# Performance work log

Measured on AMD Instinct MI355X. Metric: run time of the kernel, lower is better.

Reference implementation:

```python
import jax, jax.numpy as jnp
import numpy as np

EPS = 1e-5
N, E, IN, H, EA, T, L = 20000, 80000, 64, 32, 32, 64, 3


def graph_norm(h, w, b, ms):
    # PyG GraphNorm over a single graph: per-feature mean/var over all nodes
    mean = jnp.mean(h, axis=0, keepdims=True)
    out = h - ms * mean
    var = jnp.mean(out * out, axis=0, keepdims=True)
    return out / jnp.sqrt(var + EPS) * w + b


def setup_inputs() -> dict:
    key = jax.random.key(0)
    ks = jax.random.split(key, 24)
    s = 0.05
    inp = {
        'x': jax.random.normal(ks[0], (N, IN), jnp.float32),
        'edge_attr': jax.random.uniform(ks[1], (E, EA), dtype=jnp.float32),
        'edge_index': jax.random.randint(ks[2], (2, E), 0, N, jnp.int32),
        # initial projection in_dim -> hidden
        'init_W': jax.random.normal(ks[3], (IN, H), jnp.float32) * s,
        'init_b': jnp.zeros((H,), jnp.float32),
        # per-layer edge MLP: edge_attr_dim -> H*H (then ReLU)
        'edge_mlp_W': jax.random.normal(ks[4], (L, EA, H * H), jnp.float32) * s,
        'edge_mlp_b': jnp.zeros((L, H * H), jnp.float32),
        # NNConv root weight and bias
        'root_W': jax.random.normal(ks[5], (L, H, H), jnp.float32) * s,
        'root_b': jnp.zeros((L, H), jnp.float32),
        # per-layer GraphNorm params
        'gn_w': jnp.ones((L, H), jnp.float32),
        'gn_b': jnp.zeros((L, H), jnp.float32),
        'gn_ms': jnp.ones((L, H), jnp.float32),
        # per-layer dense transition: 2H -> H
        'trans_W': jax.random.normal(ks[6], (L, 2 * H, H), jnp.float32) * s,
        'trans_b': jnp.zeros((L, H), jnp.float32),
        # final transition H -> T and final GraphNorm
        'final_W': jax.random.normal(ks[7], (H, T), jnp.float32) * s,
        'final_b': jnp.zeros((T,), jnp.float32),
        'fgn_w': jnp.ones((T,), jnp.float32),
        'fgn_b': jnp.zeros((T,), jnp.float32),
        'fgn_ms': jnp.ones((T,), jnp.float32),
    }
    return inp


def reference(x, edge_attr, edge_index, init_W, init_b, edge_mlp_W, edge_mlp_b,
              root_W, root_b, gn_w, gn_b, gn_ms, trans_W, trans_b,
              final_W, final_b, fgn_w, fgn_b, fgn_ms):
    src, dst = edge_index[0], edge_index[1]
    n_nodes = x.shape[0]
    h = x @ init_W + init_b  # [N, H]
    for i in range(L):
        # edge-conditioned per-edge weight matrices [E, H, H]
        ew = jax.nn.relu(edge_attr @ edge_mlp_W[i] + edge_mlp_b[i]).reshape(-1, H, H)
        # gather source node feats, per-edge matmul, scatter-add to targets
        msg = jnp.einsum('ei,eio->eo', h[src], ew)  # [E, H]
        agg = jax.ops.segment_sum(msg, dst, num_segments=n_nodes)
        conv = agg + h @ root_W[i] + root_b[i]
        # GraphNorm + ReLU + residual (in_channels == out_channels)
        hc = jax.nn.relu(graph_norm(conv, gn_w[i], gn_b[i], gn_ms[i])) + h
        # dense transition on [h, h_conv]
        h = jax.nn.relu(jnp.concatenate([h, hc], axis=1) @ trans_W[i] + trans_b[i])
    out = h @ final_W + final_b
    return jax.nn.relu(graph_norm(out, fgn_w, fgn_b, fgn_ms))
```

## Files before the change

kernel.cpp:

```cpp
#include <hip/hip_runtime.h>

namespace {

constexpr int kN  = 20000;
constexpr int kE  = 80000;
constexpr int kIn = 64;
constexpr int kH  = 32;
constexpr int kEA = 32;
constexpr int kT  = 64;
constexpr int kL  = 3;
constexpr float kEps = 1e-5f;

typedef __attribute__((ext_vector_type(8))) short bf16x8;
typedef __attribute__((ext_vector_type(4))) float f32x4;

__device__ inline unsigned short f2bf(float f) {
  unsigned u = __builtin_bit_cast(unsigned, f);
  unsigned r = (u + 0x7fff + ((u >> 16) & 1)) >> 16;
  return (unsigned short)r;
}
__device__ inline float bf2f(unsigned short s) {
  unsigned u = ((unsigned)s) << 16;
  return __builtin_bit_cast(float, u);
}

__global__ __launch_bounds__(256) void hist_dst(const int* __restrict__ ei,
                                                int* __restrict__ cnt) {
  const int e = blockIdx.x * 256 + threadIdx.x;
  if (e < kE) atomicAdd(&cnt[ei[kE + e]], 1);
}

__global__ __launch_bounds__(1024) void scan_nodes(const int* __restrict__ cnt,
                                                   int* __restrict__ off,
                                                   int* __restrict__ cursor) {
  __shared__ int wsum[16];
  __shared__ int woff[16];
  const int tid = threadIdx.x, lane = tid & 63, wid = tid >> 6;
  constexpr int CH = 20;
  const int base = tid * CH;
  int v[CH];
  int s = 0;
#pragma unroll
  for (int j = 0; j < CH; ++j) {
    const int i = base + j;
    const int c = (i < kN) ? cnt[i] : 0;
    v[j] = s;
    s += c;
  }
  int x = s;
#pragma unroll
  for (int d = 1; d < 64; d <<= 1) {
    int y = __shfl_up(x, d);
    if (lane >= d) x += y;
  }
  if (lane == 63) wsum[wid] = x;
  __syncthreads();
  if (tid < 16) {
    int t = wsum[tid];
    int xx = t;
#pragma unroll
    for (int d = 1; d < 16; d <<= 1) {
      int y = __shfl_up(xx, d);
      if (tid >= d) xx += y;
    }
    woff[tid] = xx - t;
  }
  __syncthreads();
  const int thrbase = woff[wid] + (x - s);
#pragma unroll
  for (int j = 0; j < CH; ++j) {
    const int i = base + j;
    if (i < kN) {
      off[i] = thrbase + v[j];
      cursor[i] = thrbase + v[j];
    }
  }
}

__global__ __launch_bounds__(256) void place_edges(const int* __restrict__ ei,
                                                   int* __restrict__ cursor,
                                                   int* __restrict__ pos) {
  const int e = blockIdx.x * 256 + threadIdx.x;
  if (e < kE) pos[e] = atomicAdd(&cursor[ei[kE + e]], 1);
}

__global__ __launch_bounds__(256) void pack_w(const float* __restrict__ emW,
                                              unsigned short* __restrict__ wbf) {
  const int idx = blockIdx.x * 256 + threadIdx.x;
  if (idx >= kL * 64 * 64) return;
  const int lane = idx & 63, ct = (idx >> 6) & 63, l = idx >> 12;
  const int k0 = (lane >> 4) * 8, c = ct * 16 + (lane & 15);
  const float* W = emW + (size_t)l * kEA * kH * kH;
  unsigned out[4];
#pragma unroll
  for (int p = 0; p < 4; ++p) {
    unsigned lo = f2bf(W[(size_t)(k0 + 2 * p) * (kH * kH) + c]);
    unsigned hi = f2bf(W[(size_t)(k0 + 2 * p + 1) * (kH * kH) + c]);
    out[p] = lo | (hi << 16);
  }
  *reinterpret_cast<uint4*>(wbf + (size_t)idx * 8) =
      make_uint4(out[0], out[1], out[2], out[3]);
}

__global__ __launch_bounds__(64) void init_proj(
    const float* __restrict__ x, const float* __restrict__ W,
    const float* __restrict__ b, float* __restrict__ h) {
  __shared__ float Wl[kIn * kH];
  __shared__ float bl[kH];
  const int tid = threadIdx.x;
  {
    const float4* Ws = reinterpret_cast<const float4*>(W);
    float4* Wd = reinterpret_cast<float4*>(Wl);
    for (int j = tid; j < kIn * kH / 4; j += 64) Wd[j] = Ws[j];
  }
  if (tid < kH) bl[tid] = b[tid];
  __syncthreads();
  const int node = blockIdx.x * 64 + tid;
  if (node >= kN) return;
  float xr[kIn];
  const float4* xp = reinterpret_cast<const float4*>(x + (size_t)node * kIn);
#pragma unroll
  for (int k4 = 0; k4 < kIn / 4; ++k4) {
    float4 v = xp[k4];
    xr[k4 * 4 + 0] = v.x; xr[k4 * 4 + 1] = v.y;
    xr[k4 * 4 + 2] = v.z; xr[k4 * 4 + 3] = v.w;
  }
  float* hp = h + (size_t)node * kH;
#pragma unroll
  for (int o = 0; o < kH; ++o) {
    float acc = bl[o];
#pragma unroll
    for (int k = 0; k < kIn; ++k) acc = fmaf(xr[k], Wl[k * kH + o], acc);
    hp[o] = acc;
  }
}

constexpr int HP  = 40;
constexpr int MPW = 36;
__global__ __launch_bounds__(256) void edge_msg_mfma(
    const float* __restrict__ attr, const int* __restrict__ ei,
    const int* __restrict__ pos, const float* __restrict__ h,
    const unsigned short* __restrict__ wbf, const float* __restrict__ bm,
    float* __restrict__ msg_buf) {
  __shared__ float bml[kH * kH];
  __shared__ unsigned short hbuf[4][32 * HP];
  __shared__ float mbuf[4][32 * MPW];
  const int tid = threadIdx.x;
  const int wv = tid >> 6, lane = tid & 63;
  const int lr = lane & 15, lg = lane >> 4;
  const int base = (blockIdx.x * 4 + wv) * 32;

  for (int j = tid; j < kH * kH; j += 256) bml[j] = bm[j];

  bf16x8 AfA, AfB;
  {
    const float4* ap = reinterpret_cast<const float4*>(
        attr + (size_t)(base + lr) * kEA + lg * 8);
    float4 a0 = ap[0], a1 = ap[1];
    AfA[0] = (short)f2bf(a0.x); AfA[1] = (short)f2bf(a0.y);
    AfA[2] = (short)f2bf(a0.z); AfA[3] = (short)f2bf(a0.w);
    AfA[4] = (short)f2bf(a1.x); AfA[5] = (short)f2bf(a1.y);
    AfA[6] = (short)f2bf(a1.z); AfA[7] = (short)f2bf(a1.w);
    const float4* bp = reinterpret_cast<const float4*>(
        attr + (size_t)(base + 16 + lr) * kEA + lg * 8);
    float4 b0 = bp[0], b1 = bp[1];
    AfB[0] = (short)f2bf(b0.x); AfB[1] = (short)f2bf(b0.y);
    AfB[2] = (short)f2bf(b0.z); AfB[3] = (short)f2bf(b0.w);
    AfB[4] = (short)f2bf(b1.x); AfB[5] = (short)f2bf(b1.y);
    AfB[6] = (short)f2bf(b1.z); AfB[7] = (short)f2bf(b1.w);
  }

  for (int c = lane; c < 128; c += 64) {
    const int er = c >> 2, q = c & 3;
    const int src = ei[base + er];
    const float4* hp4 =
        reinterpret_cast<const float4*>(h + (size_t)src * kH + q * 8);
    float4 h0 = hp4[0], h1 = hp4[1];
    uint2 p0 = make_uint2(f2bf(h0.x) | ((unsigned)f2bf(h0.y) << 16),
                          f2bf(h0.z) | ((unsigned)f2bf(h0.w) << 16));
    uint2 p1 = make_uint2(f2bf(h1.x) | ((unsigned)f2bf(h1.y) << 16),
                          f2bf(h1.z) | ((unsigned)f2bf(h1.w) << 16));
    *reinterpret_cast<uint2*>(&hbuf[wv][0] + er * HP + q * 8) = p0;
    *reinterpret_cast<uint2*>(&hbuf[wv][0] + er * HP + q * 8 + 4) = p1;
  }

  __syncthreads();

  float maA[4][2] = {{0.f, 0.f}, {0.f, 0.f}, {0.f, 0.f}, {0.f, 0.f}};
  float maB[4][2] = {{0.f, 0.f}, {0.f, 0.f}, {0.f, 0.f}, {0.f, 0.f}};
  const unsigned short* hrow = &hbuf[wv][0];

#pragma unroll
  for (int g = 0; g < 4; ++g) {
    bf16x8 hA0 = *reinterpret_cast<const bf16x8*>(hrow + (lg * 4 + 0) * HP + g * 8);
    bf16x8 hA1 = *reinterpret_cast<const bf16x8*>(hrow + (lg * 4 + 1) * HP + g * 8);
    bf16x8 hA2 = *reinterpret_cast<const bf16x8*>(hrow + (lg * 4 + 2) * HP + g * 8);
    bf16x8 hA3 = *reinterpret_cast<const bf16x8*>(hrow + (lg * 4 + 3) * HP + g * 8);
    bf16x8 hB0 = *reinterpret_cast<const bf16x8*>(hrow + (16 + lg * 4 + 0) * HP + g * 8);
    bf16x8 hB1 = *reinterpret_cast<const bf16x8*>(hrow + (16 + lg * 4 + 1) * HP + g * 8);
    bf16x8 hB2 = *reinterpret_cast<const bf16x8*>(hrow + (16 + lg * 4 + 2) * HP + g * 8);
    bf16x8 hB3 = *reinterpret_cast<const bf16x8*>(hrow + (16 + lg * 4 + 3) * HP + g * 8);
#pragma unroll
    for (int i8 = 0; i8 < 8; ++i8) {
      const int il = g * 8 + i8;
      bf16x8 B0 = *reinterpret_cast<const bf16x8*>(
          wbf + ((size_t)(il * 2 + 0) * 64 + lane) * 8);
      bf16x8 B1 = *reinterpret_cast<const bf16x8*>(
          wbf + ((size_t)(il * 2 + 1) * 64 + lane) * 8);
      const float b0 = bml[il * kH + lr];
      const float b1 = bml[il * kH + 16 + lr];
      f32x4 c0A, c1A, c0B, c1B;
      c0A[0] = b0; c0A[1] = b0; c0A[2] = b0; c0A[3] = b0;
      c1A[0] = b1; c1A[1] = b1; c1A[2] = b1; c1A[3] = b1;
      c0B = c0A; c1B = c1A;
      c0A = __builtin_amdgcn_mfma_f32_16x16x32_bf16(AfA, B0, c0A, 0, 0, 0);
      c1A = __builtin_amdgcn_mfma_f32_16x16x32_bf16(AfA, B1, c1A, 0, 0, 0);
      c0B = __builtin_amdgcn_mfma_f32_16x16x32_bf16(AfB, B0, c0B, 0, 0, 0);
      c1B = __builtin_amdgcn_mfma_f32_16x16x32_bf16(AfB, B1, c1B, 0, 0, 0);
      {
        const float h0 = bf2f((unsigned short)hA0[i8]);
        const float h1 = bf2f((unsigned short)hA1[i8]);
        const float h2 = bf2f((unsigned short)hA2[i8]);
        const float h3 = bf2f((unsigned short)hA3[i8]);
        maA[0][0] = fmaf(fmaxf(c0A[0], 0.f), h0, maA[0][0]);
        maA[1][0] = fmaf(fmaxf(c0A[1], 0.f), h1, maA[1][0]);
        maA[2][0] = fmaf(fmaxf(c0A[2], 0.f), h2, maA[2][0]);
        maA[3][0] = fmaf(fmaxf(c0A[3], 0.f), h3, maA[3][0]);
        maA[0][1] = fmaf(fmaxf(c1A[0], 0.f), h0, maA[0][1]);
        maA[1][1] = fmaf(fmaxf(c1A[1], 0.f), h1, maA[1][1]);
        maA[2][1] = fmaf(fmaxf(c1A[2], 0.f), h2, maA[2][1]);
        maA[3][1] = fmaf(fmaxf(c1A[3], 0.f), h3, maA[3][1]);
      }
      {
        const float h0 = bf2f((unsigned short)hB0[i8]);
        const float h1 = bf2f((unsigned short)hB1[i8]);
        const float h2 = bf2f((unsigned short)hB2[i8]);
        const float h3 = bf2f((unsigned short)hB3[i8]);
        maB[0][0] = fmaf(fmaxf(c0B[0], 0.f), h0, maB[0][0]);
        maB[1][0] = fmaf(fmaxf(c0B[1], 0.f), h1, maB[1][0]);
        maB[2][0] = fmaf(fmaxf(c0B[2], 0.f), h2, maB[2][0]);
        maB[3][0] = fmaf(fmaxf(c0B[3], 0.f), h3, maB[3][0]);
        maB[0][1] = fmaf(fmaxf(c1B[0], 0.f), h0, maB[0][1]);
        maB[1][1] = fmaf(fmaxf(c1B[1], 0.f), h1, maB[1][1]);
        maB[2][1] = fmaf(fmaxf(c1B[2], 0.f), h2, maB[2][1]);
        maB[3][1] = fmaf(fmaxf(c1B[3], 0.f), h3, maB[3][1]);
      }
    }
  }

  float* mrow = &mbuf[wv][0];
#pragma unroll
  for (int r = 0; r < 4; ++r) {
    mrow[(lg * 4 + r) * MPW + lr] = maA[r][0];
    mrow[(lg * 4 + r) * MPW + 16 + lr] = maA[r][1];
    mrow[(16 + lg * 4 + r) * MPW + lr] = maB[r][0];
    mrow[(16 + lg * 4 + r) * MPW + 16 + lr] = maB[r][1];
  }
  for (int c = lane; c < 128; c += 64) {
    const int er = c >> 2, q = c & 3;
    const int mp = pos[base + er];
    float4 v0 = *reinterpret_cast<const float4*>(mrow + er * MPW + q * 8);
    float4 v1 = *reinterpret_cast<const float4*>(mrow + er * MPW + q * 8 + 4);
    float* orow = msg_buf + (size_t)mp * kH + q * 8;
    *reinterpret_cast<float4*>(orow) = v0;
    *reinterpret_cast<float4*>(orow + 4) = v1;
  }
}

__global__ __launch_bounds__(256) void agg_root_stats(
    const float* __restrict__ msg, const int* __restrict__ off,
    const int* __restrict__ cnt, const float* __restrict__ h,
    const float* __restrict__ W, const float* __restrict__ b,
    float* __restrict__ conv, float* __restrict__ stats) {
  __shared__ float Wl[kH * kH];
  __shared__ float bl[kH];
  __shared__ float buf[256 * (kH + 1)];
  const int tid = threadIdx.x;
  {
    const float4* Ws = reinterpret_cast<const float4*>(W);
    float4* Wd = reinterpret_cast<float4*>(Wl);
    if (tid < kH * kH / 4) Wd[tid] = Ws[tid];
  }
  if (tid < kH) bl[tid] = b[tid];
  __syncthreads();
  const int node = blockIdx.x * 256 + tid;
  const bool act = node < kN;
  float acc[kH];
#pragma unroll
  for (int o = 0; o < kH; ++o) acc[o] = 0.f;
  if (act) {
#pragma unroll
    for (int o = 0; o < kH; ++o) acc[o] = bl[o];
    const int s = off[node], c = cnt[node];
    for (int j = 0; j < c; ++j) {
      const float4* mp =
          reinterpret_cast<const float4*>(msg + (size_t)(s + j) * kH);
#pragma unroll
      for (int o4 = 0; o4 < kH / 4; ++o4) {
        float4 v = mp[o4];
        acc[o4 * 4 + 0] += v.x; acc[o4 * 4 + 1] += v.y;
        acc[o4 * 4 + 2] += v.z; acc[o4 * 4 + 3] += v.w;
      }
    }
    float hr[kH];
    const float4* hp = reinterpret_cast<const float4*>(h + (size_t)node * kH);
#pragma unroll
    for (int i4 = 0; i4 < kH / 4; ++i4) {
      float4 v = hp[i4];
      hr[i4 * 4 + 0] = v.x; hr[i4 * 4 + 1] = v.y;
      hr[i4 * 4 + 2] = v.z; hr[i4 * 4 + 3] = v.w;
    }
#pragma unroll
    for (int o = 0; o < kH; ++o) {
      float a = acc[o];
#pragma unroll
      for (int i = 0; i < kH; ++i) a = fmaf(hr[i], Wl[i * kH + o], a);
      acc[o] = a;
    }
    float* cp = conv + (size_t)node * kH;
#pragma unroll
    for (int o4 = 0; o4 < kH / 4; ++o4)
      *reinterpret_cast<float4*>(cp + o4 * 4) =
          make_float4(acc[o4 * 4], acc[o4 * 4 + 1], acc[o4 * 4 + 2],
                      acc[o4 * 4 + 3]);
  }
#pragma unroll
  for (int o = 0; o < kH; ++o) buf[tid * (kH + 1) + o] = act ? acc[o] : 0.f;
  __syncthreads();
  if (tid < kH) {
    float s = 0.f, q = 0.f;
#pragma unroll 8
    for (int r = 0; r < 256; ++r) {
      float v = buf[r * (kH + 1) + tid];
      s += v;
      q = fmaf(v, v, q);
    }
    atomicAdd(stats + tid, s);
    atomicAdd(stats + kH + tid, q);
  }
}

__global__ __launch_bounds__(64) void norm_trans(
    const float* __restrict__ conv, const float* __restrict__ stats,
    const float* __restrict__ gw, const float* __restrict__ gb,
    const float* __restrict__ gms, const float* __restrict__ Wt,
    const float* __restrict__ tb, float* __restrict__ h) {
  __shared__ float Wl[2 * kH * kH];
  __shared__ float tbl[kH];
  __shared__ float meanl[kH], rstdl[kH], gwl[kH], gbl[kH];
  const int tid = threadIdx.x;
  {
    const float4* Ws = reinterpret_cast<const float4*>(Wt);
    float4* Wd = reinterpret_cast<float4*>(Wl);
    for (int j = tid; j < 2 * kH * kH / 4; j += 64) Wd[j] = Ws[j];
  }
  if (tid < kH) {
    tbl[tid] = tb[tid];
    float m = stats[tid] * (1.f / kN);
    float q = stats[kH + tid] * (1.f / kN);
    float msv = gms[tid];
    float var = q - m * m * msv * (2.f - msv);
    meanl[tid] = msv * m;
    rstdl[tid] = rsqrtf(var + kEps);
    gwl[tid] = gw[tid];
    gbl[tid] = gb[tid];
  }
  __syncthreads();
  const int node = blockIdx.x * 64 + tid;
  if (node >= kN) return;
  float in_[2 * kH];
  const float* hp = h + (size_t)node * kH;
  const float* cp = conv + (size_t)node * kH;
#pragma unroll
  for (int i = 0; i < kH; ++i) in_[i] = hp[i];
#pragma unroll
  for (int o = 0; o < kH; ++o) {
    float v = cp[o];
    in_[kH + o] =
        fmaxf((v - meanl[o]) * rstdl[o] * gwl[o] + gbl[o], 0.f) + in_[o];
  }
  float* hw = h + (size_t)node * kH;
#pragma unroll
  for (int o = 0; o < kH; ++o) {
    float acc = tbl[o];
#pragma unroll
    for (int k = 0; k < 2 * kH; ++k) acc = fmaf(in_[k], Wl[k * kH + o], acc);
    hw[o] = fmaxf(acc, 0.f);
  }
}

__global__ __launch_bounds__(64) void final_lin(
    const float* __restrict__ h, const float* __restrict__ W,
    const float* __restrict__ b, float* __restrict__ out,
    float* __restrict__ stats) {
  __shared__ float Wl[kH * kT];
  __shared__ float bl[kT];
  __shared__ float buf[64 * (kT + 1)];
  const int tid = threadIdx.x;
  {
    const float4* Ws = reinterpret_cast<const float4*>(W);
    float4* Wd = reinterpret_cast<float4*>(Wl);
    for (int j = tid; j < kH * kT / 4; j += 64) Wd[j] = Ws[j];
  }
  if (tid < kT) bl[tid] = b[tid];
  __syncthreads();
  const int node = blockIdx.x * 64 + tid;
  const bool act = node < kN;
  float hr[kH];
  if (act) {
    const float4* hp = reinterpret_cast<const float4*>(h + (size_t)node * kH);
#pragma unroll
    for (int i4 = 0; i4 < kH / 4; ++i4) {
      float4 v = hp[i4];
      hr[i4 * 4 + 0] = v.x; hr[i4 * 4 + 1] = v.y;
      hr[i4 * 4 + 2] = v.z; hr[i4 * 4 + 3] = v.w;
    }
  } else {
#pragma unroll
    for (int i = 0; i < kH; ++i) hr[i] = 0.f;
  }
  float* op = out + (size_t)node * kT;
#pragma unroll
  for (int o = 0; o < kT; ++o) {
    float acc = 0.f;
    if (act) {
      acc = bl[o];
#pragma unroll
      for (int i = 0; i < kH; ++i) acc = fmaf(hr[i], Wl[i * kT + o], acc);
      op[o] = acc;
    }
    buf[tid * (kT + 1) + o] = act ? acc : 0.f;
  }
  __syncthreads();
  if (tid < kT) {
    float s = 0.f, q = 0.f;
#pragma unroll 8
    for (int r = 0; r < 64; ++r) {
      float v = buf[r * (kT + 1) + tid];
      s += v;
      q = fmaf(v, v, q);
    }
    atomicAdd(stats + tid, s);
    atomicAdd(stats + kT + tid, q);
  }
}

__global__ __launch_bounds__(64) void final_norm(
    const float* __restrict__ stats, const float* __restrict__ w,
    const float* __restrict__ b, const float* __restrict__ ms,
    float* __restrict__ out) {
  __shared__ float meanl[kT], rstdl[kT], wl2[kT], bl2[kT];
  const int tid = threadIdx.x;
  if (tid < kT) {
    float m = stats[tid] * (1.f / kN);
    float q = stats[kT + tid] * (1.f / kN);
    float msv = ms[tid];
    float var = q - m * m * msv * (2.f - msv);
    meanl[tid] = msv * m;
    rstdl[tid] = rsqrtf(var + kEps);
    wl2[tid] = w[tid];
    bl2[tid] = b[tid];
  }
  __syncthreads();
  const int node = blockIdx.x * 64 + tid;
  if (node >= kN) return;
  float* op = out + (size_t)node * kT;
#pragma unroll
  for (int o4 = 0; o4 < kT / 4; ++o4) {
    float4 v = *reinterpret_cast<const float4*>(op + o4 * 4);
    float r[4] = {v.x, v.y, v.z, v.w};
#pragma unroll
    for (int j = 0; j < 4; ++j) {
      int o = o4 * 4 + j;
      r[j] = fmaxf((r[j] - meanl[o]) * rstdl[o] * wl2[o] + bl2[o], 0.f);
    }
    *reinterpret_cast<float4*>(op + o4 * 4) =
        make_float4(r[0], r[1], r[2], r[3]);
  }
}

}

extern "C" void kernel_launch(void* const* d_in, const int* in_sizes, int n_in,
                              void* d_out, int out_size, void* d_ws,
                              size_t ws_size, hipStream_t stream) {
  const float* x     = (const float*)d_in[0];
  const float* eattr = (const float*)d_in[1];
  const int*   eidx  = (const int*)d_in[2];
  const float* initW = (const float*)d_in[3];
  const float* initb = (const float*)d_in[4];
  const float* emW   = (const float*)d_in[5];
  const float* emb   = (const float*)d_in[6];
  const float* rW    = (const float*)d_in[7];
  const float* rb    = (const float*)d_in[8];
  const float* gnw   = (const float*)d_in[9];
  const float* gnb   = (const float*)d_in[10];
  const float* gnms  = (const float*)d_in[11];
  const float* tW    = (const float*)d_in[12];
  const float* tb    = (const float*)d_in[13];
  const float* fW    = (const float*)d_in[14];
  const float* fb    = (const float*)d_in[15];
  const float* fgw   = (const float*)d_in[16];
  const float* fgb   = (const float*)d_in[17];
  const float* fgms  = (const float*)d_in[18];
  float* out = (float*)d_out;

  float* h     = (float*)d_ws;
  float* conv  = h + (size_t)kN * kH;
  float* stats = conv + (size_t)kN * kH;
  float* msg   = stats + 512;
  unsigned short* wbf = (unsigned short*)(msg + (size_t)kE * kH);
  int* cnt    = (int*)(wbf + (size_t)kL * 64 * 64 * 8);
  int* off    = cnt + kN;
  int* cursor = off + kN;
  int* pos    = cursor + kN;

  const int node64  = (kN + 63) / 64;
  const int node256 = (kN + 255) / 256;
  const int edgeBlocks = kE / 128;

  hipMemsetAsync(cnt, 0, kN * sizeof(int), stream);
  hipMemsetAsync(stats, 0, 512 * sizeof(float), stream);
  hist_dst<<<(kE + 255) / 256, 256, 0, stream>>>(eidx, cnt);
  scan_nodes<<<1, 1024, 0, stream>>>(cnt, off, cursor);
  place_edges<<<(kE + 255) / 256, 256, 0, stream>>>(eidx, cursor, pos);

  pack_w<<<kL * 64 * 64 / 256, 256, 0, stream>>>(emW, wbf);
  init_proj<<<node64, 64, 0, stream>>>(x, initW, initb, h);
  for (int l = 0; l < kL; ++l) {
    float* st = stats + l * 128;
    edge_msg_mfma<<<edgeBlocks, 256, 0, stream>>>(
        eattr, eidx, pos, h, wbf + (size_t)l * 64 * 64 * 8,
        emb + (size_t)l * kH * kH, msg);
    agg_root_stats<<<node256, 256, 0, stream>>>(
        msg, off, cnt, h, rW + (size_t)l * kH * kH, rb + l * kH, conv, st);
    norm_trans<<<node64, 64, 0, stream>>>(
        conv, st, gnw + l * kH, gnb + l * kH, gnms + l * kH,
        tW + (size_t)l * 2 * kH * kH, tb + l * kH, h);
  }
  final_lin<<<node64, 64, 0, stream>>>(h, fW, fb, out, stats + 3 * 128);
  final_norm<<<node64, 64, 0, stream>>>(stats + 3 * 128, fgw, fgb, fgms, out);
}
```

Measured before the change: 238.5 us.

## Remap node kernels to one thread per output feature with shuffle broadcasts

The node-level kernels (init_proj, agg_root_stats, norm_trans, final_lin, final_norm) switch from one thread per node with large per-thread register arrays to one lane per output feature. Groups of 32 (or 64) lanes handle a node, and input features are broadcast with __shfl. Global loads and stores become coalesced across lanes, register pressure drops, and the per-block stats reduction moves from a large padded shared buffer to shared-memory atomics. In exchange, each node's edge aggregation loop now runs per lane, and the shuffle-based inner product adds cross-lane traffic.

```diff
diff --git a/kernel.cpp b/kernel.cpp
--- a/kernel.cpp
+++ b/kernel.cpp
@@ -102,7 +102,7 @@
       make_uint4(out[0], out[1], out[2], out[3]);
 }
 
-__global__ __launch_bounds__(64) void init_proj(
+__global__ __launch_bounds__(256) void init_proj(
     const float* __restrict__ x, const float* __restrict__ W,
     const float* __restrict__ b, float* __restrict__ h) {
   __shared__ float Wl[kIn * kH];
@@ -111,27 +111,23 @@
   {
     const float4* Ws = reinterpret_cast<const float4*>(W);
     float4* Wd = reinterpret_cast<float4*>(Wl);
-    for (int j = tid; j < kIn * kH / 4; j += 64) Wd[j] = Ws[j];
+    for (int j = tid; j < kIn * kH / 4; j += 256) Wd[j] = Ws[j];
   }
   if (tid < kH) bl[tid] = b[tid];
   __syncthreads();
-  const int node = blockIdx.x * 64 + tid;
-  if (node >= kN) return;
-  float xr[kIn];
-  const float4* xp = reinterpret_cast<const float4*>(x + (size_t)node * kIn);
-#pragma unroll
-  for (int k4 = 0; k4 < kIn / 4; ++k4) {
-    float4 v = xp[k4];
-    xr[k4 * 4 + 0] = v.x; xr[k4 * 4 + 1] = v.y;
-    xr[k4 * 4 + 2] = v.z; xr[k4 * 4 + 3] = v.w;
-  }
-  float* hp = h + (size_t)node * kH;
-#pragma unroll
-  for (int o = 0; o < kH; ++o) {
+  const int hw = tid >> 5, o = tid & 31;
+#pragma unroll
+  for (int k = 0; k < 4; ++k) {
+    const int node = blockIdx.x * 32 + hw + 8 * k;
+    const float xa = x[(size_t)node * kIn + o];
+    const float xb = x[(size_t)node * kIn + 32 + o];
     float acc = bl[o];
 #pragma unroll
-    for (int k = 0; k < kIn; ++k) acc = fmaf(xr[k], Wl[k * kH + o], acc);
-    hp[o] = acc;
+    for (int i = 0; i < 32; ++i) {
+      acc = fmaf(__shfl(xa, i, 32), Wl[i * kH + o], acc);
+      acc = fmaf(__shfl(xb, i, 32), Wl[(32 + i) * kH + o], acc);
+    }
+    h[(size_t)node * kH + o] = acc;
   }
 }
 
@@ -274,7 +270,7 @@
     float* __restrict__ conv, float* __restrict__ stats) {
   __shared__ float Wl[kH * kH];
   __shared__ float bl[kH];
-  __shared__ float buf[256 * (kH + 1)];
+  __shared__ float ssum[2 * kH];
   const int tid = threadIdx.x;
   {
     const float4* Ws = reinterpret_cast<const float4*>(W);
@@ -282,65 +278,31 @@
     if (tid < kH * kH / 4) Wd[tid] = Ws[tid];
   }
   if (tid < kH) bl[tid] = b[tid];
-  __syncthreads();
-  const int node = blockIdx.x * 256 + tid;
-  const bool act = node < kN;
-  float acc[kH];
-#pragma unroll
-  for (int o = 0; o < kH; ++o) acc[o] = 0.f;
-  if (act) {
-#pragma unroll
-    for (int o = 0; o < kH; ++o) acc[o] = bl[o];
+  if (tid < 2 * kH) ssum[tid] = 0.f;
+  __syncthreads();
+  const int hw = tid >> 5, o = tid & 31;
+  float sreg = 0.f, qreg = 0.f;
+#pragma unroll
+  for (int k = 0; k < 4; ++k) {
+    const int node = blockIdx.x * 32 + hw + 8 * k;
+    float acc = bl[o];
     const int s = off[node], c = cnt[node];
-    for (int j = 0; j < c; ++j) {
-      const float4* mp =
-          reinterpret_cast<const float4*>(msg + (size_t)(s + j) * kH);
-#pragma unroll
-      for (int o4 = 0; o4 < kH / 4; ++o4) {
-        float4 v = mp[o4];
-        acc[o4 * 4 + 0] += v.x; acc[o4 * 4 + 1] += v.y;
-        acc[o4 * 4 + 2] += v.z; acc[o4 * 4 + 3] += v.w;
-      }
-    }
-    float hr[kH];
-    const float4* hp = reinterpret_cast<const float4*>(h + (size_t)node * kH);
-#pragma unroll
-    for (int i4 = 0; i4 < kH / 4; ++i4) {
-      float4 v = hp[i4];
-      hr[i4 * 4 + 0] = v.x; hr[i4 * 4 + 1] = v.y;
-      hr[i4 * 4 + 2] = v.z; hr[i4 * 4 + 3] = v.w;
-    }
-#pragma unroll
-    for (int o = 0; o < kH; ++o) {
-      float a = acc[o];
-#pragma unroll
-      for (int i = 0; i < kH; ++i) a = fmaf(hr[i], Wl[i * kH + o], a);
-      acc[o] = a;
-    }
-    float* cp = conv + (size_t)node * kH;
-#pragma unroll
-    for (int o4 = 0; o4 < kH / 4; ++o4)
-      *reinterpret_cast<float4*>(cp + o4 * 4) =
-          make_float4(acc[o4 * 4], acc[o4 * 4 + 1], acc[o4 * 4 + 2],
-                      acc[o4 * 4 + 3]);
-  }
-#pragma unroll
-  for (int o = 0; o < kH; ++o) buf[tid * (kH + 1) + o] = act ? acc[o] : 0.f;
-  __syncthreads();
-  if (tid < kH) {
-    float s = 0.f, q = 0.f;
-#pragma unroll 8
-    for (int r = 0; r < 256; ++r) {
-      float v = buf[r * (kH + 1) + tid];
-      s += v;
-      q = fmaf(v, v, q);
-    }
-    atomicAdd(stats + tid, s);
-    atomicAdd(stats + kH + tid, q);
-  }
-}
-
-__global__ __launch_bounds__(64) void norm_trans(
+    for (int j = 0; j < c; ++j) acc += msg[(size_t)(s + j) * kH + o];
+    const float hself = h[(size_t)node * kH + o];
+#pragma unroll
+    for (int i = 0; i < kH; ++i)
+      acc = fmaf(__shfl(hself, i, 32), Wl[i * kH + o], acc);
+    conv[(size_t)node * kH + o] = acc;
+    sreg += acc;
+    qreg = fmaf(acc, acc, qreg);
+  }
+  atomicAdd(&ssum[o], sreg);
+  atomicAdd(&ssum[kH + o], qreg);
+  __syncthreads();
+  if (tid < 2 * kH) atomicAdd(stats + tid, ssum[tid]);
+}
+
+__global__ __launch_bounds__(256) void norm_trans(
     const float* __restrict__ conv, const float* __restrict__ stats,
     const float* __restrict__ gw, const float* __restrict__ gb,
     const float* __restrict__ gms, const float* __restrict__ Wt,
@@ -352,7 +314,7 @@
   {
     const float4* Ws = reinterpret_cast<const float4*>(Wt);
     float4* Wd = reinterpret_cast<float4*>(Wl);
-    for (int j = tid; j < 2 * kH * kH / 4; j += 64) Wd[j] = Ws[j];
+    for (int j = tid; j < 2 * kH * kH / 4; j += 256) Wd[j] = Ws[j];
   }
   if (tid < kH) {
     tbl[tid] = tb[tid];
@@ -366,86 +328,61 @@
     gbl[tid] = gb[tid];
   }
   __syncthreads();
-  const int node = blockIdx.x * 64 + tid;
-  if (node >= kN) return;
-  float in_[2 * kH];
-  const float* hp = h + (size_t)node * kH;
-  const float* cp = conv + (size_t)node * kH;
-#pragma unroll
-  for (int i = 0; i < kH; ++i) in_[i] = hp[i];
-#pragma unroll
-  for (int o = 0; o < kH; ++o) {
-    float v = cp[o];
-    in_[kH + o] =
-        fmaxf((v - meanl[o]) * rstdl[o] * gwl[o] + gbl[o], 0.f) + in_[o];
-  }
-  float* hw = h + (size_t)node * kH;
-#pragma unroll
-  for (int o = 0; o < kH; ++o) {
+  const int hw = tid >> 5, o = tid & 31;
+#pragma unroll
+  for (int k = 0; k < 4; ++k) {
+    const int node = blockIdx.x * 32 + hw + 8 * k;
+    const float hv = h[(size_t)node * kH + o];
+    const float cv = conv[(size_t)node * kH + o];
+    const float hc =
+        fmaxf((cv - meanl[o]) * rstdl[o] * gwl[o] + gbl[o], 0.f) + hv;
     float acc = tbl[o];
 #pragma unroll
-    for (int k = 0; k < 2 * kH; ++k) acc = fmaf(in_[k], Wl[k * kH + o], acc);
-    hw[o] = fmaxf(acc, 0.f);
-  }
-}
-
-__global__ __launch_bounds__(64) void final_lin(
+    for (int i = 0; i < kH; ++i) {
+      acc = fmaf(__shfl(hv, i, 32), Wl[i * kH + o], acc);
+      acc = fmaf(__shfl(hc, i, 32), Wl[(kH + i) * kH + o], acc);
+    }
+    h[(size_t)node * kH + o] = fmaxf(acc, 0.f);
+  }
+}
+
+__global__ __launch_bounds__(256) void final_lin(
     const float* __restrict__ h, const float* __restrict__ W,
     const float* __restrict__ b, float* __restrict__ out,
     float* __restrict__ stats) {
   __shared__ float Wl[kH * kT];
   __shared__ float bl[kT];
-  __shared__ float buf[64 * (kT + 1)];
+  __shared__ float ssum[2 * kT];
   const int tid = threadIdx.x;
   {
     const float4* Ws = reinterpret_cast<const float4*>(W);
     float4* Wd = reinterpret_cast<float4*>(Wl);
-    for (int j = tid; j < kH * kT / 4; j += 64) Wd[j] = Ws[j];
+    for (int j = tid; j < kH * kT / 4; j += 256) Wd[j] = Ws[j];
   }
   if (tid < kT) bl[tid] = b[tid];
-  __syncthreads();
-  const int node = blockIdx.x * 64 + tid;
-  const bool act = node < kN;
-  float hr[kH];
-  if (act) {
-    const float4* hp = reinterpret_cast<const float4*>(h + (size_t)node * kH);
-#pragma unroll
-    for (int i4 = 0; i4 < kH / 4; ++i4) {
-      float4 v = hp[i4];
-      hr[i4 * 4 + 0] = v.x; hr[i4 * 4 + 1] = v.y;
-      hr[i4 * 4 + 2] = v.z; hr[i4 * 4 + 3] = v.w;
-    }
-  } else {
-#pragma unroll
-    for (int i = 0; i < kH; ++i) hr[i] = 0.f;
-  }
-  float* op = out + (size_t)node * kT;
-#pragma unroll
-  for (int o = 0; o < kT; ++o) {
-    float acc = 0.f;
-    if (act) {
-      acc = bl[o];
-#pragma unroll
-      for (int i = 0; i < kH; ++i) acc = fmaf(hr[i], Wl[i * kT + o], acc);
-      op[o] = acc;
-    }
-    buf[tid * (kT + 1) + o] = act ? acc : 0.f;
-  }
-  __syncthreads();
-  if (tid < kT) {
-    float s = 0.f, q = 0.f;
-#pragma unroll 8
-    for (int r = 0; r < 64; ++r) {
-      float v = buf[r * (kT + 1) + tid];
-      s += v;
-      q = fmaf(v, v, q);
-    }
-    atomicAdd(stats + tid, s);
-    atomicAdd(stats + kT + tid, q);
-  }
-}
-
-__global__ __launch_bounds__(64) void final_norm(
+  if (tid < 2 * kT) ssum[tid] = 0.f;
+  __syncthreads();
+  const int wv = tid >> 6, o = tid & 63;
+  float sreg = 0.f, qreg = 0.f;
+#pragma unroll
+  for (int k = 0; k < 8; ++k) {
+    const int node = blockIdx.x * 32 + wv + 4 * k;
+    const float hself = h[(size_t)node * kH + (o & 31)];
+    float acc = bl[o];
+#pragma unroll
+    for (int i = 0; i < kH; ++i)
+      acc = fmaf(__shfl(hself, i, 32), Wl[i * kT + o], acc);
+    out[(size_t)node * kT + o] = acc;
+    sreg += acc;
+    qreg = fmaf(acc, acc, qreg);
+  }
+  atomicAdd(&ssum[o], sreg);
+  atomicAdd(&ssum[kT + o], qreg);
+  __syncthreads();
+  if (tid < 2 * kT) atomicAdd(stats + tid, ssum[tid]);
+}
+
+__global__ __launch_bounds__(256) void final_norm(
     const float* __restrict__ stats, const float* __restrict__ w,
     const float* __restrict__ b, const float* __restrict__ ms,
     float* __restrict__ out) {
@@ -462,21 +399,17 @@
     bl2[tid] = b[tid];
   }
   __syncthreads();
-  const int node = blockIdx.x * 64 + tid;
-  if (node >= kN) return;
-  float* op = out + (size_t)node * kT;
-#pragma unroll
-  for (int o4 = 0; o4 < kT / 4; ++o4) {
-    float4 v = *reinterpret_cast<const float4*>(op + o4 * 4);
-    float r[4] = {v.x, v.y, v.z, v.w};
-#pragma unroll
-    for (int j = 0; j < 4; ++j) {
-      int o = o4 * 4 + j;
-      r[j] = fmaxf((r[j] - meanl[o]) * rstdl[o] * wl2[o] + bl2[o], 0.f);
-    }
-    *reinterpret_cast<float4*>(op + o4 * 4) =
-        make_float4(r[0], r[1], r[2], r[3]);
-  }
+  const int idx = blockIdx.x * 256 + tid;
+  const int f = idx * 4;
+  const int c0 = f & 63;
+  float4 v = *reinterpret_cast<const float4*>(out + f);
+  float r[4] = {v.x, v.y, v.z, v.w};
+#pragma unroll
+  for (int j = 0; j < 4; ++j) {
+    const int o = c0 + j;
+    r[j] = fmaxf((r[j] - meanl[o]) * rstdl[o] * wl2[o] + bl2[o], 0.f);
+  }
+  *reinterpret_cast<float4*>(out + f) = make_float4(r[0], r[1], r[2], r[3]);
 }
 
 }
@@ -515,8 +448,7 @@
   int* cursor = off + kN;
   int* pos    = cursor + kN;
 
-  const int node64  = (kN + 63) / 64;
-  const int node256 = (kN + 255) / 256;
+  const int nodeHW  = kN / 32;
   const int edgeBlocks = kE / 128;
 
   hipMemsetAsync(cnt, 0, kN * sizeof(int), stream);
@@ -526,18 +458,19 @@
   place_edges<<<(kE + 255) / 256, 256, 0, stream>>>(eidx, cursor, pos);
 
   pack_w<<<kL * 64 * 64 / 256, 256, 0, stream>>>(emW, wbf);
-  init_proj<<<node64, 64, 0, stream>>>(x, initW, initb, h);
+  init_proj<<<nodeHW, 256, 0, stream>>>(x, initW, initb, h);
   for (int l = 0; l < kL; ++l) {
     float* st = stats + l * 128;
     edge_msg_mfma<<<edgeBlocks, 256, 0, stream>>>(
         eattr, eidx, pos, h, wbf + (size_t)l * 64 * 64 * 8,
         emb + (size_t)l * kH * kH, msg);
-    agg_root_stats<<<node256, 256, 0, stream>>>(
+    agg_root_stats<<<nodeHW, 256, 0, stream>>>(
         msg, off, cnt, h, rW + (size_t)l * kH * kH, rb + l * kH, conv, st);
-    norm_trans<<<node64, 64, 0, stream>>>(
+    norm_trans<<<nodeHW, 256, 0, stream>>>(
         conv, st, gnw + l * kH, gnb + l * kH, gnms + l * kH,
         tW + (size_t)l * 2 * kH * kH, tb + l * kH, h);
   }
-  final_lin<<<node64, 64, 0, stream>>>(h, fW, fb, out, stats + 3 * 128);
-  final_norm<<<node64, 64, 0, stream>>>(stats + 3 * 128, fgw, fgb, fgms, out);
-}
+  final_lin<<<nodeHW, 256, 0, stream>>>(h, fW, fb, out, stats + 3 * 128);
+  final_norm<<<kN * kT / 1024, 256, 0, stream>>>(stats + 3 * 128, fgw, fgb,
+                                                 fgms, out);
+}
```

Measured after the change: 287.9 us. +20.7%, slower.
